# Kernel optimization log

Measured on AMD Instinct MI355X. Metric: run time of the kernel, lower is better.

The kernel has to match this reference:

```python
import jax, jax.numpy as jnp
import numpy as np

N = 50000      # nodes
E = 800000     # edges (before self loops)
D = 128        # node feat dim (in = hidden = out)
R_IN = 64      # edge feat in
R_OUT = 64     # edge feat out


def setup_inputs() -> dict:
    key = jax.random.key(0)
    ks = jax.random.split(key, 10)
    src = jax.random.randint(ks[0], (E,), 0, N, dtype=jnp.int32)
    dst = jax.random.randint(ks[1], (E,), 0, N, dtype=jnp.int32)
    x = jax.random.normal(ks[2], (N, D), jnp.float32)
    text_h = jax.random.normal(ks[3], (E, R_IN), jnp.float32)
    s = 1.0 / np.sqrt(D)
    W1 = jax.random.normal(ks[4], (D, D), jnp.float32) * s
    b1 = jnp.zeros((D,), jnp.float32)
    W2 = jax.random.normal(ks[5], (D, D), jnp.float32) * s
    b2 = jnp.zeros((D,), jnp.float32)
    sr = 1.0 / np.sqrt(R_IN)
    relW = jax.random.normal(ks[6], (R_IN, R_OUT), jnp.float32) * sr
    relb = jnp.zeros((R_OUT,), jnp.float32)
    return {"src": src, "dst": dst, "x": x, "text_h": text_h,
            "W1": W1, "b1": b1, "W2": W2, "b2": b2,
            "relW": relW, "relb": relb}


def _graph_conv(h, src, dst, norm_src, norm_dst, W, b, n):
    # DGL GraphConv, norm='both': scale src, gather, segment-sum to dst, scale dst, linear, relu
    h = h * norm_src                                   # [N, D]
    agg = jax.ops.segment_sum(h[src], dst, num_segments=n)  # [N, D]
    h = agg * norm_dst
    return jax.nn.relu(h @ W + b)


def reference(src, dst, x, text_h, W1, b1, W2, b2, relW, relb):
    n = x.shape[0]
    loop = jnp.arange(n, dtype=src.dtype)
    src_a = jnp.concatenate([src, loop])               # add_self_loop
    dst_a = jnp.concatenate([dst, loop])
    ones = jnp.ones(src_a.shape[0], x.dtype)
    out_deg = jax.ops.segment_sum(ones, src_a, num_segments=n)
    in_deg = jax.ops.segment_sum(ones, dst_a, num_segments=n)
    norm_src = (out_deg ** -0.5)[:, None]              # >=1 thanks to self loops
    norm_dst = (in_deg ** -0.5)[:, None]
    h = _graph_conv(x, src_a, dst_a, norm_src, norm_dst, W1, b1, n)
    h = _graph_conv(h, src_a, dst_a, norm_src, norm_dst, W2, b2, n)
    # apply_edges: rel_linear on text_h (self-loop edges get zero-filled text_h)
    text_all = jnp.concatenate([text_h, jnp.zeros((n, text_h.shape[1]), text_h.dtype)])
    e_h = text_all @ relW + relb                       # [E+N, R_OUT]
    # apply_nodes: activation applied once more
    h = jax.nn.relu(h)
    return h, e_h
```

## Files before the change

### kernel.cpp

```cpp
#include <hip/hip_runtime.h>

constexpr int D = 128;
constexpr int R = 64;
constexpr int CAP = 64;
constexpr int OVF_CAP = 65536;
constexpr int TPAD = 68;

typedef float floatx4 __attribute__((ext_vector_type(4)));
typedef short bf16x8 __attribute__((ext_vector_type(8)));
typedef float f32x4 __attribute__((ext_vector_type(4)));

static __device__ __forceinline__ float4 f4fma(float a, float4 w, float4 c) {
  c.x = fmaf(a, w.x, c.x); c.y = fmaf(a, w.y, c.y);
  c.z = fmaf(a, w.z, c.z); c.w = fmaf(a, w.w, c.w);
  return c;
}

static __device__ __forceinline__ void nt_store4(float4 v, float* p) {
  floatx4 q; q.x = v.x; q.y = v.y; q.z = v.z; q.w = v.w;
  __builtin_nontemporal_store(q, (floatx4*)p);
}

static __device__ __forceinline__ float selk(float4 a, int kk) {
  return (kk == 0) ? a.x : (kk == 1) ? a.y : (kk == 2) ? a.z : a.w;
}

static __device__ __forceinline__ unsigned pack_bf16x2(float lo, float hi) {
  unsigned ulo = __float_as_uint(lo), uhi = __float_as_uint(hi);
  ulo += 0x7FFFu + ((ulo >> 16) & 1u);
  uhi += 0x7FFFu + ((uhi >> 16) & 1u);
  return (ulo >> 16) | (uhi & 0xFFFF0000u);
}
static __device__ __forceinline__ short f2bf(float f) {
  unsigned u = __float_as_uint(f);
  u += 0x7FFFu + ((u >> 16) & 1u);
  return (short)(u >> 16);
}
static __device__ __forceinline__ float bf_lo(unsigned u) { return __uint_as_float(u << 16); }
static __device__ __forceinline__ float bf_hi(unsigned u) { return __uint_as_float(u & 0xFFFF0000u); }

__global__ void k_init(int* deg_out, int* cursor, int* ovf_cnt, int n) {
  int i = blockIdx.x * blockDim.x + threadIdx.x;
  if (i < n) { deg_out[i] = 1; cursor[i] = 0; }
  if (i == 0) ovf_cnt[0] = 0;
}

__global__ void k_fill(const int* __restrict__ src, const int* __restrict__ dst,
                       int* deg_out, int* cursor, int* bucket,
                       int* ovf_cnt, int2* ovf, int e) {
  int i = blockIdx.x * blockDim.x + threadIdx.x;
  if (i >= e) return;
  int d = dst[i], s = src[i];
  atomicAdd(&deg_out[s], 1);
  int slot = atomicAdd(&cursor[d], 1);
  if (slot < CAP) bucket[(size_t)d * CAP + slot] = s;
  else {
    int oi = atomicAdd(ovf_cnt, 1);
    if (oi < OVF_CAP) ovf[oi] = make_int2(s, d);
  }
}

__global__ void k_norm(const int* __restrict__ deg_out, const int* __restrict__ cursor,
                       float* ns, float* nd, int n) {
  int i = blockIdx.x * blockDim.x + threadIdx.x;
  if (i < n) {
    ns[i] = rsqrtf((float)deg_out[i]);
    nd[i] = rsqrtf((float)(cursor[i] + 1));
  }
}

__global__ __launch_bounds__(256) void k_prep(const float* __restrict__ X,
                                              const float* __restrict__ ns,
                                              uint4* __restrict__ xs, int n16) {
  int idx = blockIdx.x * 256 + threadIdx.x;
  if (idx >= n16) return;
  int row = idx >> 4, g = idx & 15;
  const float4* xp = (const float4*)(X + (size_t)row * D + g * 8);
  float4 a = xp[0], b = xp[1];
  float s = ns[row];
  uint4 o;
  o.x = pack_bf16x2(a.x * s, a.y * s);
  o.y = pack_bf16x2(a.z * s, a.w * s);
  o.z = pack_bf16x2(b.x * s, b.y * s);
  o.w = pack_bf16x2(b.z * s, b.w * s);
  xs[(size_t)row * 16 + g] = o;
}

__global__ __launch_bounds__(256) void k_agg_b(const unsigned* __restrict__ XS,
                                               const int* __restrict__ cursor,
                                               const int* __restrict__ bucket,
                                               float* __restrict__ agg, int n) {
  int g = threadIdx.x >> 5, lane = threadIdx.x & 31;
  int v = blockIdx.x * 8 + g;
  if (v >= n) return;
  float4 acc;
  {
    uint2 u = ((const uint2*)(XS + (size_t)v * 64))[lane];
    acc.x = bf_lo(u.x); acc.y = bf_hi(u.x); acc.z = bf_lo(u.y); acc.w = bf_hi(u.y);
  }
  int cnt = min(cursor[v], CAP);
  const int* bk = bucket + (size_t)v * CAP;
  int i = 0;
  for (; i + 4 <= cnt; i += 4) {
    int s0 = bk[i], s1 = bk[i + 1], s2 = bk[i + 2], s3 = bk[i + 3];
    uint2 u0 = ((const uint2*)(XS + (size_t)s0 * 64))[lane];
    uint2 u1 = ((const uint2*)(XS + (size_t)s1 * 64))[lane];
    uint2 u2 = ((const uint2*)(XS + (size_t)s2 * 64))[lane];
    uint2 u3 = ((const uint2*)(XS + (size_t)s3 * 64))[lane];
    acc.x += bf_lo(u0.x) + bf_lo(u1.x) + bf_lo(u2.x) + bf_lo(u3.x);
    acc.y += bf_hi(u0.x) + bf_hi(u1.x) + bf_hi(u2.x) + bf_hi(u3.x);
    acc.z += bf_lo(u0.y) + bf_lo(u1.y) + bf_lo(u2.y) + bf_lo(u3.y);
    acc.w += bf_hi(u0.y) + bf_hi(u1.y) + bf_hi(u2.y) + bf_hi(u3.y);
  }
  for (; i < cnt; ++i) {
    int s0 = bk[i];
    uint2 u0 = ((const uint2*)(XS + (size_t)s0 * 64))[lane];
    acc.x += bf_lo(u0.x); acc.y += bf_hi(u0.x);
    acc.z += bf_lo(u0.y); acc.w += bf_hi(u0.y);
  }
  ((float4*)(agg + (size_t)v * D))[lane] = acc;
}

__global__ __launch_bounds__(128) void k_ovf_b(const unsigned* __restrict__ XS,
                                               const int* __restrict__ ovf_cnt,
                                               const int2* __restrict__ ovf,
                                               float* agg) {
  int m = min(ovf_cnt[0], OVF_CAP);
  int t = threadIdx.x;
  for (int i = blockIdx.x; i < m; i += gridDim.x) {
    int2 e = ovf[i];
    unsigned u = XS[(size_t)e.x * 64 + (t >> 1)];
    float f = (t & 1) ? bf_hi(u) : bf_lo(u);
    atomicAdd(&agg[(size_t)e.y * D + t], f);
  }
}

__global__ __launch_bounds__(256) void k_gemm_relu(const float* __restrict__ A,
                                                   const float* __restrict__ ndv,
                                                   const float* __restrict__ W,
                                                   const float* __restrict__ bias,
                                                   const float* __restrict__ post,
                                                   float* __restrict__ outf,
                                                   unsigned* __restrict__ outb,
                                                   int n) {
  __shared__ float Wl[D * D];
  int t = threadIdx.x;
  for (int i = t; i < (D * D) / 4; i += 256) ((float4*)Wl)[i] = ((const float4*)W)[i];
  __syncthreads();

  int ct = t & 15, rg = t >> 4;
  int c0 = ct << 2;
  int row0 = blockIdx.x * 64;

  float4 bb0 = *(const float4*)(bias + c0);
  float4 bb1 = *(const float4*)(bias + c0 + 64);

  int r[4]; const float4* Ap[4];
#pragma unroll
  for (int m = 0; m < 4; ++m) {
    r[m] = row0 + rg + 16 * m;
    int rc = (r[m] < n) ? r[m] : (n - 1);
    Ap[m] = (const float4*)(A + (size_t)rc * D);
  }

  float4 acc[4][2];
#pragma unroll
  for (int m = 0; m < 4; ++m) {
    acc[m][0] = make_float4(0.f, 0.f, 0.f, 0.f);
    acc[m][1] = make_float4(0.f, 0.f, 0.f, 0.f);
  }

#pragma unroll 8
  for (int k4 = 0; k4 < 32; ++k4) {
    float4 a0 = Ap[0][k4], a1 = Ap[1][k4], a2 = Ap[2][k4], a3 = Ap[3][k4];
    const float* wbase = Wl + (k4 << 9) + c0;
#pragma unroll
    for (int kk = 0; kk < 4; ++kk) {
      float4 w0 = *(const float4*)(wbase + (kk << 7));
      float4 w1 = *(const float4*)(wbase + (kk << 7) + 64);
      float e0 = selk(a0, kk), e1 = selk(a1, kk), e2 = selk(a2, kk), e3 = selk(a3, kk);
      acc[0][0] = f4fma(e0, w0, acc[0][0]); acc[0][1] = f4fma(e0, w1, acc[0][1]);
      acc[1][0] = f4fma(e1, w0, acc[1][0]); acc[1][1] = f4fma(e1, w1, acc[1][1]);
      acc[2][0] = f4fma(e2, w0, acc[2][0]); acc[2][1] = f4fma(e2, w1, acc[2][1]);
      acc[3][0] = f4fma(e3, w0, acc[3][0]); acc[3][1] = f4fma(e3, w1, acc[3][1]);
    }
  }

#pragma unroll
  for (int m = 0; m < 4; ++m) {
    if (r[m] < n) {
      float ndr = ndv[r[m]];
      float4 o0, o1;
      o0.x = fmaxf(fmaf(acc[m][0].x, ndr, bb0.x), 0.f);
      o0.y = fmaxf(fmaf(acc[m][0].y, ndr, bb0.y), 0.f);
      o0.z = fmaxf(fmaf(acc[m][0].z, ndr, bb0.z), 0.f);
      o0.w = fmaxf(fmaf(acc[m][0].w, ndr, bb0.w), 0.f);
      o1.x = fmaxf(fmaf(acc[m][1].x, ndr, bb1.x), 0.f);
      o1.y = fmaxf(fmaf(acc[m][1].y, ndr, bb1.y), 0.f);
      o1.z = fmaxf(fmaf(acc[m][1].z, ndr, bb1.z), 0.f);
      o1.w = fmaxf(fmaf(acc[m][1].w, ndr, bb1.w), 0.f);
      if (outb) {
        float ps = post[r[m]];
        uint2 p0, p1;
        p0.x = pack_bf16x2(o0.x * ps, o0.y * ps);
        p0.y = pack_bf16x2(o0.z * ps, o0.w * ps);
        p1.x = pack_bf16x2(o1.x * ps, o1.y * ps);
        p1.y = pack_bf16x2(o1.z * ps, o1.w * ps);
        *(uint2*)(outb + (size_t)r[m] * 64 + (c0 >> 1)) = p0;
        *(uint2*)(outb + (size_t)r[m] * 64 + (c0 >> 1) + 32) = p1;
      } else {
        *(float4*)(outf + (size_t)r[m] * D + c0) = o0;
        *(float4*)(outf + (size_t)r[m] * D + c0 + 64) = o1;
      }
    }
  }
}

__global__ __launch_bounds__(256) void k_rel_mfma(const float* __restrict__ T,
                                                  const float* __restrict__ Wr,
                                                  const float* __restrict__ br,
                                                  float* __restrict__ out,
                                                  int e, int ntot) {
  __shared__ float Tl[128 * TPAD];
  int t = threadIdx.x;
  int tile = blockIdx.x;
  const float4 z4 = make_float4(0.f, 0.f, 0.f, 0.f);

  float4 pre[8];
#pragma unroll
  for (int j = 0; j < 8; ++j) {
    int idx = t + 256 * j, rr = idx >> 4, c4 = idx & 15;
    int grow = tile * 128 + rr;
    pre[j] = (grow < e) ? ((const float4*)T)[(size_t)grow * 16 + c4] : z4;
  }

  int l = t & 63;
  int wid = t >> 6;
  int lr = l & 15;
  int kg = l >> 4;
  bf16x8 bfrag[4][2];
#pragma unroll
  for (int ct = 0; ct < 4; ++ct)
#pragma unroll
    for (int h = 0; h < 2; ++h) {
      const float* wp = Wr + (size_t)(h * 32 + kg * 8) * 64 + ct * 16 + lr;
#pragma unroll
      for (int i = 0; i < 8; ++i) bfrag[ct][h][i] = f2bf(wp[(size_t)i * 64]);
    }
  float bias[4];
#pragma unroll
  for (int ct = 0; ct < 4; ++ct) bias[ct] = br[ct * 16 + lr];

#pragma unroll
  for (int j = 0; j < 8; ++j) {
    int idx = t + 256 * j, rr = idx >> 4, c4 = idx & 15;
    *(float4*)&Tl[rr * TPAD + (c4 << 2)] = pre[j];
  }
  __syncthreads();

  f32x4 acc2[2][4];
#pragma unroll
  for (int g = 0; g < 2; ++g) {
    int lrow = wid * 32 + g * 16 + lr;
    const float* tp = &Tl[lrow * TPAD];
    bf16x8 afrag[2];
#pragma unroll
    for (int h = 0; h < 2; ++h) {
      float4 a0 = *(const float4*)(tp + h * 32 + kg * 8);
      float4 a1 = *(const float4*)(tp + h * 32 + kg * 8 + 4);
      afrag[h][0] = f2bf(a0.x); afrag[h][1] = f2bf(a0.y);
      afrag[h][2] = f2bf(a0.z); afrag[h][3] = f2bf(a0.w);
      afrag[h][4] = f2bf(a1.x); afrag[h][5] = f2bf(a1.y);
      afrag[h][6] = f2bf(a1.z); afrag[h][7] = f2bf(a1.w);
    }
#pragma unroll
    for (int ct = 0; ct < 4; ++ct) {
      f32x4 acc;
      acc[0] = bias[ct]; acc[1] = bias[ct]; acc[2] = bias[ct]; acc[3] = bias[ct];
      acc = __builtin_amdgcn_mfma_f32_16x16x32_bf16(afrag[0], bfrag[ct][0], acc, 0, 0, 0);
      acc = __builtin_amdgcn_mfma_f32_16x16x32_bf16(afrag[1], bfrag[ct][1], acc, 0, 0, 0);
      acc2[g][ct] = acc;
    }
  }

  __syncthreads();
#pragma unroll
  for (int g = 0; g < 2; ++g)
#pragma unroll
    for (int ct = 0; ct < 4; ++ct)
#pragma unroll
      for (int r = 0; r < 4; ++r)
        Tl[(wid * 32 + g * 16 + kg * 4 + r) * TPAD + ct * 16 + lr] = acc2[g][ct][r];
  __syncthreads();

#pragma unroll
  for (int j = 0; j < 8; ++j) {
    int idx = t + 256 * j, rr = idx >> 4, c4 = idx & 15;
    int grow = tile * 128 + rr;
    if (grow < ntot)
      nt_store4(*(float4*)&Tl[rr * TPAD + (c4 << 2)], out + (size_t)grow * R + (c4 << 2));
  }
}

extern "C" void kernel_launch(void* const* d_in, const int* in_sizes, int n_in,
                              void* d_out, int out_size, void* d_ws, size_t ws_size,
                              hipStream_t stream) {
  const int*   src  = (const int*)d_in[0];
  const int*   dst  = (const int*)d_in[1];
  const float* x    = (const float*)d_in[2];
  const float* text = (const float*)d_in[3];
  const float* W1   = (const float*)d_in[4];
  const float* b1   = (const float*)d_in[5];
  const float* W2   = (const float*)d_in[6];
  const float* b2   = (const float*)d_in[7];
  const float* relW = (const float*)d_in[8];
  const float* relb = (const float*)d_in[9];

  const int E = in_sizes[0];
  const int N = in_sizes[2] / D;

  float* outH = (float*)d_out;
  float* outE = outH + (size_t)N * D;

  char* w = (char*)d_ws;
  auto alloc = [&](size_t bytes) -> void* {
    void* p = (void*)w;
    w += (bytes + 255) & ~(size_t)255;
    return p;
  };
  int*      deg_out  = (int*)alloc((size_t)N * 4);
  int*      cursor   = (int*)alloc((size_t)N * 4);
  float*    norm_src = (float*)alloc((size_t)N * 4);
  float*    norm_dst = (float*)alloc((size_t)N * 4);
  int*      ovf_cnt  = (int*)alloc(256);
  int2*     ovf      = (int2*)alloc((size_t)OVF_CAP * 8);
  int*      bucket   = (int*)alloc((size_t)N * CAP * 4);
  float*    agg      = (float*)alloc((size_t)N * D * 4);
  unsigned* xs       = (unsigned*)alloc((size_t)N * 64 * 4);
  unsigned* h1p      = (unsigned*)alloc((size_t)N * 64 * 4);

  int nbN = (N + 255) / 256;
  int nbE = (E + 255) / 256;

  k_init<<<nbN, 256, 0, stream>>>(deg_out, cursor, ovf_cnt, N);
  k_fill<<<nbE, 256, 0, stream>>>(src, dst, deg_out, cursor, bucket, ovf_cnt, ovf, E);
  k_norm<<<nbN, 256, 0, stream>>>(deg_out, cursor, norm_src, norm_dst, N);

  k_prep<<<(N * 16 + 255) / 256, 256, 0, stream>>>(x, norm_src, (uint4*)xs, N * 16);
  k_agg_b<<<(N + 7) / 8, 256, 0, stream>>>(xs, cursor, bucket, agg, N);
  k_ovf_b<<<64, 128, 0, stream>>>(xs, ovf_cnt, ovf, agg);
  k_gemm_relu<<<(N + 63) / 64, 256, 0, stream>>>(agg, norm_dst, W1, b1, norm_src,
                                                 nullptr, h1p, N);

  k_agg_b<<<(N + 7) / 8, 256, 0, stream>>>(h1p, cursor, bucket, agg, N);
  k_ovf_b<<<64, 128, 0, stream>>>(h1p, ovf_cnt, ovf, agg);
  k_gemm_relu<<<(N + 63) / 64, 256, 0, stream>>>(agg, norm_dst, W2, b2, nullptr,
                                                 outH, nullptr, N);

  int ntot = E + N;
  int nBlk = (ntot + 127) / 128;
  k_rel_mfma<<<nBlk, 256, 0, stream>>>(text, relW, relb, outE, E, ntot);
}
```

Measured before the change: 336.2 us.

## Interleave edge linear tiles with aggregation blocks and fold norm into prep

Splits the independent edge rel-linear GEMM into two halves and co-schedules each half with a gather aggregation pass in a single combined kernel, alternating block roles. The aim is to overlap the latency-bound random gathers with the streaming, bandwidth-heavy edge GEMM. The rel tile shrinks from 128 to 64 rows, and the norm computation is folded into the prep kernel, removing one launch. The cost is more LDS per aggregation block, which can lower occupancy, plus some redundant rsqrt work in prep.

Result: slower. 361.7 us (+7.6%).

```diff
diff --git a/kernel.cpp b/kernel.cpp
--- a/kernel.cpp
+++ b/kernel.cpp
@@ -5,6 +5,7 @@
 constexpr int CAP = 64;
 constexpr int OVF_CAP = 65536;
 constexpr int TPAD = 68;
+constexpr int RELR = 64;
 
 typedef float floatx4 __attribute__((ext_vector_type(4)));
 typedef short bf16x8 __attribute__((ext_vector_type(8)));
@@ -60,65 +61,28 @@
   }
 }
 
-__global__ void k_norm(const int* __restrict__ deg_out, const int* __restrict__ cursor,
-                       float* ns, float* nd, int n) {
-  int i = blockIdx.x * blockDim.x + threadIdx.x;
-  if (i < n) {
-    ns[i] = rsqrtf((float)deg_out[i]);
-    nd[i] = rsqrtf((float)(cursor[i] + 1));
-  }
-}
-
 __global__ __launch_bounds__(256) void k_prep(const float* __restrict__ X,
-                                              const float* __restrict__ ns,
+                                              const int* __restrict__ deg_out,
+                                              const int* __restrict__ cursor,
+                                              float* __restrict__ ns,
+                                              float* __restrict__ nd,
                                               uint4* __restrict__ xs, int n16) {
   int idx = blockIdx.x * 256 + threadIdx.x;
   if (idx >= n16) return;
   int row = idx >> 4, g = idx & 15;
+  float s = rsqrtf((float)deg_out[row]);
+  if (g == 0) {
+    ns[row] = s;
+    nd[row] = rsqrtf((float)(cursor[row] + 1));
+  }
   const float4* xp = (const float4*)(X + (size_t)row * D + g * 8);
   float4 a = xp[0], b = xp[1];
-  float s = ns[row];
   uint4 o;
   o.x = pack_bf16x2(a.x * s, a.y * s);
   o.y = pack_bf16x2(a.z * s, a.w * s);
   o.z = pack_bf16x2(b.x * s, b.y * s);
   o.w = pack_bf16x2(b.z * s, b.w * s);
   xs[(size_t)row * 16 + g] = o;
-}
-
-__global__ __launch_bounds__(256) void k_agg_b(const unsigned* __restrict__ XS,
-                                               const int* __restrict__ cursor,
-                                               const int* __restrict__ bucket,
-                                               float* __restrict__ agg, int n) {
-  int g = threadIdx.x >> 5, lane = threadIdx.x & 31;
-  int v = blockIdx.x * 8 + g;
-  if (v >= n) return;
-  float4 acc;
-  {
-    uint2 u = ((const uint2*)(XS + (size_t)v * 64))[lane];
-    acc.x = bf_lo(u.x); acc.y = bf_hi(u.x); acc.z = bf_lo(u.y); acc.w = bf_hi(u.y);
-  }
-  int cnt = min(cursor[v], CAP);
-  const int* bk = bucket + (size_t)v * CAP;
-  int i = 0;
-  for (; i + 4 <= cnt; i += 4) {
-    int s0 = bk[i], s1 = bk[i + 1], s2 = bk[i + 2], s3 = bk[i + 3];
-    uint2 u0 = ((const uint2*)(XS + (size_t)s0 * 64))[lane];
-    uint2 u1 = ((const uint2*)(XS + (size_t)s1 * 64))[lane];
-    uint2 u2 = ((const uint2*)(XS + (size_t)s2 * 64))[lane];
-    uint2 u3 = ((const uint2*)(XS + (size_t)s3 * 64))[lane];
-    acc.x += bf_lo(u0.x) + bf_lo(u1.x) + bf_lo(u2.x) + bf_lo(u3.x);
-    acc.y += bf_hi(u0.x) + bf_hi(u1.x) + bf_hi(u2.x) + bf_hi(u3.x);
-    acc.z += bf_lo(u0.y) + bf_lo(u1.y) + bf_lo(u2.y) + bf_lo(u3.y);
-    acc.w += bf_hi(u0.y) + bf_hi(u1.y) + bf_hi(u2.y) + bf_hi(u3.y);
-  }
-  for (; i < cnt; ++i) {
-    int s0 = bk[i];
-    uint2 u0 = ((const uint2*)(XS + (size_t)s0 * 64))[lane];
-    acc.x += bf_lo(u0.x); acc.y += bf_hi(u0.x);
-    acc.z += bf_lo(u0.y); acc.w += bf_hi(u0.y);
-  }
-  ((float4*)(agg + (size_t)v * D))[lane] = acc;
 }
 
 __global__ __launch_bounds__(128) void k_ovf_b(const unsigned* __restrict__ XS,
@@ -216,21 +180,69 @@
   }
 }
 
-__global__ __launch_bounds__(256) void k_rel_mfma(const float* __restrict__ T,
-                                                  const float* __restrict__ Wr,
-                                                  const float* __restrict__ br,
-                                                  float* __restrict__ out,
-                                                  int e, int ntot) {
-  __shared__ float Tl[128 * TPAD];
+__global__ __launch_bounds__(256) void k_mix(const unsigned* __restrict__ XS,
+                                             const int* __restrict__ cursor,
+                                             const int* __restrict__ bucket,
+                                             float* __restrict__ agg, int n,
+                                             const float* __restrict__ T,
+                                             const float* __restrict__ Wr,
+                                             const float* __restrict__ br,
+                                             float* __restrict__ outE,
+                                             int e, int ntot,
+                                             int nA, int nR, int relBase) {
+  __shared__ float Tl[RELR * TPAD];
+  int b = blockIdx.x;
+  int nPair = 2 * (nA < nR ? nA : nR);
+  bool isRel; int idx;
+  if (b < nPair) { isRel = (b & 1) != 0; idx = b >> 1; }
+  else {
+    int rr = b - nPair;
+    if (nA < nR) { isRel = true;  idx = nA + rr; }
+    else         { isRel = false; idx = nR + rr; }
+  }
   int t = threadIdx.x;
-  int tile = blockIdx.x;
+
+  if (!isRel) {
+    int g = t >> 5, lane = t & 31;
+    int v = idx * 8 + g;
+    if (v >= n) return;
+    float4 acc;
+    {
+      uint2 u = ((const uint2*)(XS + (size_t)v * 64))[lane];
+      acc.x = bf_lo(u.x); acc.y = bf_hi(u.x); acc.z = bf_lo(u.y); acc.w = bf_hi(u.y);
+    }
+    int cnt = min(cursor[v], CAP);
+    const int* bk = bucket + (size_t)v * CAP;
+    int i = 0;
+    for (; i + 4 <= cnt; i += 4) {
+      int s0 = bk[i], s1 = bk[i + 1], s2 = bk[i + 2], s3 = bk[i + 3];
+      uint2 u0 = ((const uint2*)(XS + (size_t)s0 * 64))[lane];
+      uint2 u1 = ((const uint2*)(XS + (size_t)s1 * 64))[lane];
+      uint2 u2 = ((const uint2*)(XS + (size_t)s2 * 64))[lane];
+      uint2 u3 = ((const uint2*)(XS + (size_t)s3 * 64))[lane];
+      acc.x += bf_lo(u0.x) + bf_lo(u1.x) + bf_lo(u2.x) + bf_lo(u3.x);
+      acc.y += bf_hi(u0.x) + bf_hi(u1.x) + bf_hi(u2.x) + bf_hi(u3.x);
+      acc.z += bf_lo(u0.y) + bf_lo(u1.y) + bf_lo(u2.y) + bf_lo(u3.y);
+      acc.w += bf_hi(u0.y) + bf_hi(u1.y) + bf_hi(u2.y) + bf_hi(u3.y);
+    }
+    for (; i < cnt; ++i) {
+      int s0 = bk[i];
+      uint2 u0 = ((const uint2*)(XS + (size_t)s0 * 64))[lane];
+      acc.x += bf_lo(u0.x); acc.y += bf_hi(u0.x);
+      acc.z += bf_lo(u0.y); acc.w += bf_hi(u0.y);
+    }
+    ((float4*)(agg + (size_t)v * D))[lane] = acc;
+    return;
+  }
+
+  int tile = relBase + idx;
   const float4 z4 = make_float4(0.f, 0.f, 0.f, 0.f);
 
-  float4 pre[8];
-#pragma unroll
-  for (int j = 0; j < 8; ++j) {
-    int idx = t + 256 * j, rr = idx >> 4, c4 = idx & 15;
-    int grow = tile * 128 + rr;
+  float4 pre[4];
+#pragma unroll
+  for (int j = 0; j < 4; ++j) {
+    int q = t + 256 * j, rr = q >> 4, c4 = q & 15;
+    int grow = tile * RELR + rr;
     pre[j] = (grow < e) ? ((const float4*)T)[(size_t)grow * 16 + c4] : z4;
   }
 
@@ -252,53 +264,48 @@
   for (int ct = 0; ct < 4; ++ct) bias[ct] = br[ct * 16 + lr];
 
 #pragma unroll
-  for (int j = 0; j < 8; ++j) {
-    int idx = t + 256 * j, rr = idx >> 4, c4 = idx & 15;
+  for (int j = 0; j < 4; ++j) {
+    int q = t + 256 * j, rr = q >> 4, c4 = q & 15;
     *(float4*)&Tl[rr * TPAD + (c4 << 2)] = pre[j];
   }
   __syncthreads();
 
-  f32x4 acc2[2][4];
-#pragma unroll
-  for (int g = 0; g < 2; ++g) {
-    int lrow = wid * 32 + g * 16 + lr;
-    const float* tp = &Tl[lrow * TPAD];
-    bf16x8 afrag[2];
-#pragma unroll
-    for (int h = 0; h < 2; ++h) {
-      float4 a0 = *(const float4*)(tp + h * 32 + kg * 8);
-      float4 a1 = *(const float4*)(tp + h * 32 + kg * 8 + 4);
-      afrag[h][0] = f2bf(a0.x); afrag[h][1] = f2bf(a0.y);
-      afrag[h][2] = f2bf(a0.z); afrag[h][3] = f2bf(a0.w);
-      afrag[h][4] = f2bf(a1.x); afrag[h][5] = f2bf(a1.y);
-      afrag[h][6] = f2bf(a1.z); afrag[h][7] = f2bf(a1.w);
-    }
-#pragma unroll
-    for (int ct = 0; ct < 4; ++ct) {
-      f32x4 acc;
-      acc[0] = bias[ct]; acc[1] = bias[ct]; acc[2] = bias[ct]; acc[3] = bias[ct];
-      acc = __builtin_amdgcn_mfma_f32_16x16x32_bf16(afrag[0], bfrag[ct][0], acc, 0, 0, 0);
-      acc = __builtin_amdgcn_mfma_f32_16x16x32_bf16(afrag[1], bfrag[ct][1], acc, 0, 0, 0);
-      acc2[g][ct] = acc;
-    }
+  int lrow = wid * 16 + lr;
+  const float* tp = &Tl[lrow * TPAD];
+  bf16x8 afrag[2];
+#pragma unroll
+  for (int h = 0; h < 2; ++h) {
+    float4 a0 = *(const float4*)(tp + h * 32 + kg * 8);
+    float4 a1 = *(const float4*)(tp + h * 32 + kg * 8 + 4);
+    afrag[h][0] = f2bf(a0.x); afrag[h][1] = f2bf(a0.y);
+    afrag[h][2] = f2bf(a0.z); afrag[h][3] = f2bf(a0.w);
+    afrag[h][4] = f2bf(a1.x); afrag[h][5] = f2bf(a1.y);
+    afrag[h][6] = f2bf(a1.z); afrag[h][7] = f2bf(a1.w);
+  }
+  f32x4 acc2[4];
+#pragma unroll
+  for (int ct = 0; ct < 4; ++ct) {
+    f32x4 acc;
+    acc[0] = bias[ct]; acc[1] = bias[ct]; acc[2] = bias[ct]; acc[3] = bias[ct];
+    acc = __builtin_amdgcn_mfma_f32_16x16x32_bf16(afrag[0], bfrag[ct][0], acc, 0, 0, 0);
+    acc = __builtin_amdgcn_mfma_f32_16x16x32_bf16(afrag[1], bfrag[ct][1], acc, 0, 0, 0);
+    acc2[ct] = acc;
   }
 
   __syncthreads();
 #pragma unroll
-  for (int g = 0; g < 2; ++g)
-#pragma unroll
-    for (int ct = 0; ct < 4; ++ct)
-#pragma unroll
-      for (int r = 0; r < 4; ++r)
-        Tl[(wid * 32 + g * 16 + kg * 4 + r) * TPAD + ct * 16 + lr] = acc2[g][ct][r];
+  for (int ct = 0; ct < 4; ++ct)
+#pragma unroll
+    for (int r = 0; r < 4; ++r)
+      Tl[(wid * 16 + kg * 4 + r) * TPAD + ct * 16 + lr] = acc2[ct][r];
   __syncthreads();
 
 #pragma unroll
-  for (int j = 0; j < 8; ++j) {
-    int idx = t + 256 * j, rr = idx >> 4, c4 = idx & 15;
-    int grow = tile * 128 + rr;
+  for (int j = 0; j < 4; ++j) {
+    int q = t + 256 * j, rr = q >> 4, c4 = q & 15;
+    int grow = tile * RELR + rr;
     if (grow < ntot)
-      nt_store4(*(float4*)&Tl[rr * TPAD + (c4 << 2)], out + (size_t)grow * R + (c4 << 2));
+      nt_store4(*(float4*)&Tl[rr * TPAD + (c4 << 2)], outE + (size_t)grow * R + (c4 << 2));
   }
 }
 
@@ -344,20 +351,26 @@
 
   k_init<<<nbN, 256, 0, stream>>>(deg_out, cursor, ovf_cnt, N);
   k_fill<<<nbE, 256, 0, stream>>>(src, dst, deg_out, cursor, bucket, ovf_cnt, ovf, E);
-  k_norm<<<nbN, 256, 0, stream>>>(deg_out, cursor, norm_src, norm_dst, N);
-
-  k_prep<<<(N * 16 + 255) / 256, 256, 0, stream>>>(x, norm_src, (uint4*)xs, N * 16);
-  k_agg_b<<<(N + 7) / 8, 256, 0, stream>>>(xs, cursor, bucket, agg, N);
+  k_prep<<<(N * 16 + 255) / 256, 256, 0, stream>>>(x, deg_out, cursor,
+                                                   norm_src, norm_dst, (uint4*)xs, N * 16);
+
+  int ntot = E + N;
+  int nRelTiles = (ntot + RELR - 1) / RELR;
+  int half1 = nRelTiles / 2;
+  int half2 = nRelTiles - half1;
+  int nA = (N + 7) / 8;
+
+  k_mix<<<nA + half1, 256, 0, stream>>>(xs, cursor, bucket, agg, N,
+                                        text, relW, relb, outE, E, ntot,
+                                        nA, half1, 0);
   k_ovf_b<<<64, 128, 0, stream>>>(xs, ovf_cnt, ovf, agg);
   k_gemm_relu<<<(N + 63) / 64, 256, 0, stream>>>(agg, norm_dst, W1, b1, norm_src,
                                                  nullptr, h1p, N);
 
-  k_agg_b<<<(N + 7) / 8, 256, 0, stream>>>(h1p, cursor, bucket, agg, N);
+  k_mix<<<nA + half2, 256, 0, stream>>>(h1p, cursor, bucket, agg, N,
+                                        text, relW, relb, outE, E, ntot,
+                                        nA, half2, half1);
   k_ovf_b<<<64, 128, 0, stream>>>(h1p, ovf_cnt, ovf, agg);
   k_gemm_relu<<<(N + 63) / 64, 256, 0, stream>>>(agg, norm_dst, W2, b2, nullptr,
                                                  outH, nullptr, N);
-
-  int ntot = E + N;
-  int nBlk = (ntot + 127) / 128;
-  k_rel_mfma<<<nBlk, 256, 0, stream>>>(text, relW, relb, outE, E, ntot);
-}
+}
```
